# Kernel tuning notes

Hardware: AMD Instinct MI355X
Metric: run time of the kernel (lower is better)

The kernel has to match this reference:

```python
import jax, jax.numpy as jnp
import numpy as np

T, B, IN, H, OUT = 512, 128, 64, 1024, 64


def _gru_layer(x, w_ih, w_hh, b_ih, b_hh):
    # x: (T, B, in_dim); w_ih: (3H, in_dim); w_hh: (3H, H); gate order: r, z, n (torch)
    gi = jnp.einsum('tbi,gi->tbg', x, w_ih) + b_ih  # (T, B, 3H) input-side gates, precomputed
    h0 = jnp.zeros((x.shape[1], w_hh.shape[1]), x.dtype)

    def step(h, gi_t):
        gh = h @ w_hh.T + b_hh                      # (B, 3H)
        ir, iz, inn = jnp.split(gi_t, 3, axis=-1)
        hr, hz, hn = jnp.split(gh, 3, axis=-1)
        r = jax.nn.sigmoid(ir + hr)
        z = jax.nn.sigmoid(iz + hz)
        n = jnp.tanh(inn + r * hn)
        h_new = (1.0 - z) * n + z * h
        return h_new, h_new

    _, out = jax.lax.scan(step, h0, gi)             # out: (T, B, H)
    return out


def setup_inputs() -> dict:
    key = jax.random.key(0)
    ks = jax.random.split(key, 11)
    s_in = 1.0 / np.sqrt(H)
    inp = {
        'x': jax.random.normal(ks[0], (T, B, IN), dtype=jnp.float32),
        'w_ih0': jax.random.uniform(ks[1], (3 * H, IN), jnp.float32, -s_in, s_in),
        'w_hh0': jax.random.uniform(ks[2], (3 * H, H), jnp.float32, -s_in, s_in),
        'b_ih0': jax.random.uniform(ks[3], (3 * H,), jnp.float32, -s_in, s_in),
        'b_hh0': jax.random.uniform(ks[4], (3 * H,), jnp.float32, -s_in, s_in),
        'w_ih1': jax.random.uniform(ks[5], (3 * H, H), jnp.float32, -s_in, s_in),
        'w_hh1': jax.random.uniform(ks[6], (3 * H, H), jnp.float32, -s_in, s_in),
        'b_ih1': jax.random.uniform(ks[7], (3 * H,), jnp.float32, -s_in, s_in),
        'b_hh1': jax.random.uniform(ks[8], (3 * H,), jnp.float32, -s_in, s_in),
        'w_lin': jax.random.uniform(ks[9], (OUT, H), jnp.float32, -s_in, s_in),
        'b_lin': jax.random.uniform(ks[10], (OUT,), jnp.float32, -s_in, s_in),
    }
    return inp


def reference(x, w_ih0, w_hh0, b_ih0, b_hh0, w_ih1, w_hh1, b_ih1, b_hh1, w_lin, b_lin):
    h1 = _gru_layer(x, w_ih0, w_hh0, b_ih0, b_hh0)   # (T, B, H)
    h2 = _gru_layer(h1, w_ih1, w_hh1, b_ih1, b_hh1)  # (T, B, H)
    out = jnp.einsum('tbh,oh->tbo', h2, w_lin) + b_lin  # time-distributed linear
    return out
```

## Files before the change

kernel.cpp:

```cpp
#include <hip/hip_runtime.h>

#define Tn  512
#define Bn  128
#define INn 64
#define Hn  1024

typedef __attribute__((ext_vector_type(8))) _Float16 f16x8;
typedef __attribute__((ext_vector_type(4))) float f32x4;
typedef unsigned short u16;

#define AGENT __HIP_MEMORY_SCOPE_AGENT

__device__ __forceinline__ u16 f2h(float f) {
  union { _Float16 h; u16 u; } v;
  v.h = (_Float16)f;
  return v.u;
}
__device__ __forceinline__ float sigmoidf_(float x) {
  return 1.0f / (1.0f + __expf(-x));
}
__device__ __forceinline__ float tanhf_(float x) {
  float e = __expf(-2.0f * fabsf(x));
  float t = (1.0f - e) / (1.0f + e);
  return copysignf(t, x);
}
__device__ __forceinline__ f32x4 mfma16(f16x8 a, f16x8 b, f32x4 c) {
  return __builtin_amdgcn_mfma_f32_16x16x32_f16(a, b, c, 0, 0, 0);
}
__device__ __forceinline__ size_t hidx(int row, int col) {
  return ((size_t)((row >> 4) * 32 + (col >> 5))) * 512 +
         ((((col >> 3) & 3) * 16 + (row & 15)) * 8) + (col & 7);
}
__device__ __forceinline__ void acq_fence() {
  __builtin_amdgcn_fence(__ATOMIC_ACQUIRE, "agent");
}
__device__ __forceinline__ void coh_store(u16* p, u16 a, u16 b) {
  __hip_atomic_store((unsigned*)p, (unsigned)a | ((unsigned)b << 16),
                     __ATOMIC_RELAXED, AGENT);
}
__device__ __forceinline__ void ldb4(f16x8 dst[4], const u16* __restrict__ h,
                                     size_t ab, int kc0) {
#pragma unroll
  for (int k = 0; k < 4; ++k)
    dst[k] = *(const f16x8*)(h + ab + (size_t)(kc0 + k) * 512);
}
__device__ __forceinline__ void fma12(f32x4 acc[3], const f16x8 b[4],
                                      const f16x8 W[3][8], int kc0) {
#pragma unroll
  for (int k = 0; k < 4; ++k) {
#pragma unroll
    for (int g = 0; g < 3; ++g)
      acc[g] = mfma16(b[k], W[g][kc0 + k], acc[g]);
  }
}

__global__ void pack_w(const float* __restrict__ s, u16* __restrict__ d, int R, int K) {
  int tid = blockIdx.x * blockDim.x + threadIdx.x;
  int total = (R * K) >> 3;
  if (tid >= total) return;
  int l = tid & 63;
  int ckc = tid >> 6;
  int nkc = K >> 5;
  int ct = ckc / nkc;
  int kc = ckc - ct * nkc;
  int row = ct * 16 + (l & 15);
  int k0 = kc * 32 + (l >> 4) * 8;
  const float* sp = s + (size_t)row * K + k0;
  float4 a = *(const float4*)sp;
  float4 b = *(const float4*)(sp + 4);
  f16x8 o;
  u16* op = (u16*)&o;
  op[0] = f2h(a.x); op[1] = f2h(a.y); op[2] = f2h(a.z); op[3] = f2h(a.w);
  op[4] = f2h(b.x); op[5] = f2h(b.y); op[6] = f2h(b.z); op[7] = f2h(b.w);
  *(f16x8*)(d + (size_t)tid * 8) = o;
}

__global__ void zero16(uint4* __restrict__ p, int n4) {
  int i = blockIdx.x * blockDim.x + threadIdx.x;
  if (i < n4) p[i] = make_uint4(0u, 0u, 0u, 0u);
}

#define PS 131072

template <bool WO>
__global__ __launch_bounds__(512, 1) void gru_main(
    const float* __restrict__ x,
    const float* __restrict__ b_ih0, const float* __restrict__ b_hh0,
    const float* __restrict__ b_ih1, const float* __restrict__ b_hh1,
    const float* __restrict__ b_lin,
    const u16* __restrict__ wih0p, const u16* __restrict__ whh0p,
    const u16* __restrict__ wih1p, const u16* __restrict__ whh1p,
    const u16* __restrict__ wlinp,
    u16* __restrict__ hA, u16* __restrict__ hB,
    float* __restrict__ out, int* __restrict__ flags) {
  extern __shared__ float lds[];

  const int blk  = blockIdx.x;
  const int tid  = threadIdx.x;
  const int w    = tid >> 6;
  const int lane = tid & 63;
  const int ln   = lane & 15;
  const int lq   = lane >> 4;
  const int layer = blk >> 7;
  const int lb   = blk & 127;
  const f32x4 vz = {0.f, 0.f, 0.f, 0.f};

  if (layer == 0) {
    const int bg  = lb >> 5;
    const int hsl = lb & 31;
    const int q   = w & 1;
    const int kg  = w >> 1;
    const int c16 = hsl * 2 + q;
    const bool kgl = (kg < 2);
    const int xm  = kg;
    f16x8 W[3][8];
#pragma unroll
    for (int g = 0; g < 3; ++g)
#pragma unroll
      for (int kc = 0; kc < 8; ++kc)
        W[g][kc] = *(const f16x8*)(whh0p + (((size_t)(g * 64 + c16) * 32 + kg * 8 + kc) * 64 + lane) * 8);
    f16x8 Wx[3][2];
    if (kgl) {
#pragma unroll
      for (int g = 0; g < 3; ++g)
#pragma unroll
        for (int kc = 0; kc < 2; ++kc)
          Wx[g][kc] = *(const f16x8*)(wih0p + (((size_t)(g * 64 + c16) * 2 + kc) * 64 + lane) * 8);
    }
    const bool is_lin = (hsl < 8);
    const int lcg = hsl & 3;
    const int lrt = hsl >> 2;
    float Blin = 0.f;
    f16x8 Wl[4];
    if (is_lin) {
      Blin = b_lin[lcg * 16 + (tid & 15)];
#pragma unroll
      for (int kc = 0; kc < 4; ++kc)
        Wl[kc] = *(const f16x8*)(wlinp + (((size_t)lcg * 32 + w * 4 + kc) * 64 + lane) * 8);
    }
    const int rm  = tid >> 8;
    const int rr  = (tid >> 4) & 15;
    const int rc2 = (tid & 15) * 2;
    const int ggr = bg * 32 + rm * 16 + rr;
    float Br[2], Bz[2], Bni[2], Bnh[2];
#pragma unroll
    for (int e = 0; e < 2; ++e) {
      const int gc = hsl * 32 + rc2 + e;
      Br[e]  = b_ih0[gc] + b_hh0[gc];
      Bz[e]  = b_ih0[Hn + gc] + b_hh0[Hn + gc];
      Bni[e] = b_ih0[2 * Hn + gc];
      Bnh[e] = b_hh0[2 * Hn + gc];
    }
    const int* pPeer = flags + ((bg << 5) + (lane & 31)) * 32;
    const int* pBp   = flags + 4096 + (((bg >> 1) << 6) + lane) * 32;
    const size_t abL = ((size_t)(bg * 2 + lrt) * 32 + w * 4) * 512 + lane * 8;
    float h0prev[2] = {0.f, 0.f};

    for (int t = 0; t <= Tn + 7; ++t) {
      f16x8 lbuf[4];
      if (t < Tn) {
        if (w == 0) {
          const bool needB = WO ? (is_lin && t >= 8) : (t >= 8);
          for (;;) {
            bool ok = true;
            if (t > 0 && __hip_atomic_load(pPeer, __ATOMIC_RELAXED, AGENT) < t) ok = false;
            if (needB && __hip_atomic_load(pBp, __ATOMIC_RELAXED, AGENT) < t - 7) ok = false;
            if (!__all(ok)) { __builtin_amdgcn_s_sleep(1); continue; }
            break;
          }
          if (!WO) acq_fence();
        }
        __syncthreads();
        const u16* Ahb = hA + (size_t)(WO ? t : ((t + 7) & 7)) * PS;
        float4 xv0, xv1, xv2, xv3;
        if (kgl) {
          const float* xr = x + ((size_t)t * Bn + bg * 32 + xm * 16 + ln) * INn + lq * 8;
          xv0 = *(const float4*)xr;        xv1 = *(const float4*)(xr + 4);
          xv2 = *(const float4*)(xr + 32); xv3 = *(const float4*)(xr + 36);
        }
        f32x4 acc0[3] = {vz, vz, vz}, acc1[3] = {vz, vz, vz};
        f16x8 b0[4], b1[4], b2[4], b3[4];
        const size_t ab0 = ((size_t)(bg * 2 + 0) * 32 + kg * 8) * 512 + lane * 8;
        const size_t ab1 = ((size_t)(bg * 2 + 1) * 32 + kg * 8) * 512 + lane * 8;
        ldb4(b0, Ahb, ab0, 0);
        ldb4(b1, Ahb, ab0, 4);
        ldb4(b2, Ahb, ab1, 0);
        ldb4(b3, Ahb, ab1, 4);
        if (is_lin && t >= 8)
          ldb4(lbuf, hB + (size_t)(WO ? (t - 7) : ((t - 8) & 7)) * PS, abL, 0);
        fma12(acc0, b0, W, 0);
        fma12(acc0, b1, W, 4);
        fma12(acc1, b2, W, 0);
        fma12(acc1, b3, W, 4);
        {
          float* Hp0 = lds + (size_t)(0 * 4 + kg) * 1680;
          float* Hp1 = lds + (size_t)(1 * 4 + kg) * 1680;
#pragma unroll
          for (int g = 0; g < 3; ++g)
#pragma unroll
            for (int i = 0; i < 4; ++i) {
              Hp0[g * 560 + (lq * 4 + i) * 35 + q * 16 + ln] = acc0[g][i];
              Hp1[g * 560 + (lq * 4 + i) * 35 + q * 16 + ln] = acc1[g][i];
            }
        }
        if (kgl) {
          f16x8 a0, a1;
          u16* a0p = (u16*)&a0;
          u16* a1p = (u16*)&a1;
          a0p[0] = f2h(xv0.x); a0p[1] = f2h(xv0.y); a0p[2] = f2h(xv0.z); a0p[3] = f2h(xv0.w);
          a0p[4] = f2h(xv1.x); a0p[5] = f2h(xv1.y); a0p[6] = f2h(xv1.z); a0p[7] = f2h(xv1.w);
          a1p[0] = f2h(xv2.x); a1p[1] = f2h(xv2.y); a1p[2] = f2h(xv2.z); a1p[3] = f2h(xv2.w);
          a1p[4] = f2h(xv3.x); a1p[5] = f2h(xv3.y); a1p[6] = f2h(xv3.z); a1p[7] = f2h(xv3.w);
          f32x4 ax[3] = {vz, vz, vz};
#pragma unroll
          for (int g = 0; g < 3; ++g) {
            ax[g] = mfma16(a0, Wx[g][0], ax[g]);
            ax[g] = mfma16(a1, Wx[g][1], ax[g]);
          }
          float* Ip = lds + 13440 + (size_t)xm * 1680;
#pragma unroll
          for (int g = 0; g < 3; ++g)
#pragma unroll
            for (int i = 0; i < 4; ++i)
              Ip[g * 560 + (lq * 4 + i) * 35 + q * 16 + ln] = ax[g][i];
        }
        __syncthreads();
        {
          u16* whp = hA + (size_t)(WO ? (t + 1) : (t & 7)) * PS;
          const size_t idx0 = hidx(ggr, hsl * 32 + rc2);
          u16 hh[2];
#pragma unroll
          for (int e = 0; e < 2; ++e) {
            const int c = rc2 + e;
            const float* Ip = lds + 13440 + (size_t)rm * 1680 + rr * 35 + c;
            float I0 = Ip[0], I1 = Ip[560], I2 = Ip[1120];
            float H0 = 0.f, H1 = 0.f, H2 = 0.f;
#pragma unroll
            for (int kgi = 0; kgi < 4; ++kgi) {
              const float* Hp = lds + (size_t)(rm * 4 + kgi) * 1680 + rr * 35 + c;
              H0 += Hp[0]; H1 += Hp[560]; H2 += Hp[1120];
            }
            float r  = sigmoidf_(I0 + H0 + Br[e]);
            float zz = sigmoidf_(I1 + H1 + Bz[e]);
            float nn = tanhf_(I2 + Bni[e] + r * (H2 + Bnh[e]));
            float hv = (1.0f - zz) * nn + zz * h0prev[e];
            h0prev[e] = hv;
            hh[e] = f2h(hv);
          }
          coh_store(whp + idx0, hh[0], hh[1]);
        }
        __syncthreads();
        if (tid == 0)
          __hip_atomic_store(flags + ((bg << 5) + hsl) * 32, t + 1, __ATOMIC_RELAXED, AGENT);
      } else if (is_lin) {
        if (w == 0) {
          while (!__all(__hip_atomic_load(pBp, __ATOMIC_RELAXED, AGENT) >= t - 7))
            __builtin_amdgcn_s_sleep(1);
          if (!WO) acq_fence();
        }
        __syncthreads();
        ldb4(lbuf, hB + (size_t)(WO ? (t - 7) : ((t - 8) & 7)) * PS, abL, 0);
      }
      if (is_lin && t >= 8) {
        const int s2 = t - 8;
        f32x4 la = vz;
#pragma unroll
        for (int k = 0; k < 4; ++k)
          la = mfma16(lbuf[k], Wl[k], la);
        __syncthreads();
        if (!WO && tid == 0)
          __hip_atomic_store(flags + 8192 + ((bg << 3) + hsl) * 32, s2 + 1, __ATOMIC_RELAXED, AGENT);
#pragma unroll
        for (int i = 0; i < 4; ++i)
          lds[(w * 16 + lq * 4 + i) * 21 + ln] = la[i];
        __syncthreads();
        if (tid < 256) {
          const int lr = (tid >> 4) & 15, lc = tid & 15;
          float s = Blin;
#pragma unroll
          for (int w8 = 0; w8 < 8; ++w8)
            s += lds[(w8 * 16 + lr) * 21 + lc];
          out[((size_t)s2 * Bn + bg * 32 + lrt * 16 + lr) * 64 + lcg * 16 + lc] = s;
        }
      }
    }
  } else {
    const int cs  = lb >> 1;
    const int rh  = lb & 1;
    const int side = w >> 2;
    const int ks  = w & 3;
    const u16* wsrc = side ? whh1p : wih1p;
    f16x8 W[3][8];
#pragma unroll
    for (int g = 0; g < 3; ++g)
#pragma unroll
      for (int kc = 0; kc < 8; ++kc)
        W[g][kc] = *(const f16x8*)(wsrc + (((size_t)(g * 64 + cs) * 32 + ks * 8 + kc) * 64 + lane) * 8);
    const int mq  = tid >> 7;
    const int er  = (tid >> 3) & 15;
    const int ec0 = (tid & 7) * 2;
    float Br2[2], Bz2[2], Bni2[2], Bnh2[2];
#pragma unroll
    for (int e = 0; e < 2; ++e) {
      const int g2 = cs * 16 + ec0 + e;
      Br2[e]  = b_ih1[g2] + b_hh1[g2];
      Bz2[e]  = b_ih1[Hn + g2] + b_hh1[Hn + g2];
      Bni2[e] = b_ih1[2 * Hn + g2];
      Bnh2[e] = b_hh1[2 * Hn + g2];
    }
    const size_t idxE = hidx(rh * 64 + mq * 16 + er, cs * 16 + ec0);
    float h1prev[2] = {0.f, 0.f};
    const int* pA = flags + ((rh << 6) + lane) * 32;
    const int* pB = flags + 4096 + ((rh << 6) + lane) * 32;
    const int* pC = flags + 8192 + ((rh << 4) + (lane & 15)) * 32;

    for (int s = 0; s < Tn; ++s) {
      if (w == 0) {
        for (;;) {
          bool ok = __hip_atomic_load(pA, __ATOMIC_RELAXED, AGENT) >= s + 1;
          if (!WO && s >= 8 && (lane & 15) == lane &&
              __hip_atomic_load(pC, __ATOMIC_RELAXED, AGENT) < s - 7) ok = false;
          if (__all(ok)) break;
          __builtin_amdgcn_s_sleep(1);
        }
        if (!WO) acq_fence();
      }
      __syncthreads();
      const u16* A1h = hA + (size_t)(WO ? (s + 1) : (s & 7)) * PS;
      const u16* A2h = hB + (size_t)(WO ? s : ((s + 7) & 7)) * PS;
      u16* whp = hB + (size_t)(WO ? (s + 1) : (s & 7)) * PS;
      const u16* Ahb = side ? A2h : A1h;
      if (side && s > 0) {
        while (!__all(__hip_atomic_load(pB, __ATOMIC_RELAXED, AGENT) >= s))
          __builtin_amdgcn_s_sleep(1);
      }
      f32x4 acc0[3] = {vz, vz, vz}, acc1[3] = {vz, vz, vz};
      f32x4 acc2[3] = {vz, vz, vz}, acc3[3] = {vz, vz, vz};
      f16x8 b0[4], b1[4], b2[4], b3[4];
      const int mA = rh * 4;
      const size_t abT0 = ((size_t)(mA + 0) * 32 + ks * 8) * 512 + lane * 8;
      const size_t abT1 = ((size_t)(mA + 1) * 32 + ks * 8) * 512 + lane * 8;
      const size_t abT2 = ((size_t)(mA + 2) * 32 + ks * 8) * 512 + lane * 8;
      const size_t abT3 = ((size_t)(mA + 3) * 32 + ks * 8) * 512 + lane * 8;
      ldb4(b0, Ahb, abT0, 0);
      ldb4(b1, Ahb, abT0, 4);
      ldb4(b2, Ahb, abT1, 0);
      ldb4(b3, Ahb, abT1, 4);
      fma12(acc0, b0, W, 0);
      ldb4(b0, Ahb, abT2, 0);
      fma12(acc0, b1, W, 4);
      ldb4(b1, Ahb, abT2, 4);
      fma12(acc1, b2, W, 0);
      ldb4(b2, Ahb, abT3, 0);
      fma12(acc1, b3, W, 4);
      ldb4(b3, Ahb, abT3, 4);
      fma12(acc2, b0, W, 0);
      fma12(acc2, b1, W, 4);
      fma12(acc3, b2, W, 0);
      fma12(acc3, b3, W, 4);
#pragma unroll
      for (int g = 0; g < 3; ++g)
#pragma unroll
        for (int i = 0; i < 4; ++i) {
          const int ro = (lq * 4 + i) * 21 + ln;
          lds[((0 * 8 + w) * 3 + g) * 336 + ro] = acc0[g][i];
          lds[((1 * 8 + w) * 3 + g) * 336 + ro] = acc1[g][i];
          lds[((2 * 8 + w) * 3 + g) * 336 + ro] = acc2[g][i];
          lds[((3 * 8 + w) * 3 + g) * 336 + ro] = acc3[g][i];
        }
      __syncthreads();
      {
        u16 hh[2];
#pragma unroll
        for (int e = 0; e < 2; ++e) {
          const int rc = ec0 + e;
          float I0 = 0.f, I1 = 0.f, I2 = 0.f, H0 = 0.f, H1 = 0.f, H2 = 0.f;
#pragma unroll
          for (int wi = 0; wi < 4; ++wi) {
            const float* P = lds + ((mq * 8 + wi) * 3) * 336 + er * 21 + rc;
            I0 += P[0]; I1 += P[336]; I2 += P[672];
          }
#pragma unroll
          for (int wi = 4; wi < 8; ++wi) {
            const float* P = lds + ((mq * 8 + wi) * 3) * 336 + er * 21 + rc;
            H0 += P[0]; H1 += P[336]; H2 += P[672];
          }
          float r  = sigmoidf_(I0 + H0 + Br2[e]);
          float zz = sigmoidf_(I1 + H1 + Bz2[e]);
          float nn = tanhf_(I2 + Bni2[e] + r * (H2 + Bnh2[e]));
          float hv = (1.0f - zz) * nn + zz * h1prev[e];
          h1prev[e] = hv;
          hh[e] = f2h(hv);
        }
        coh_store(whp + idxE, hh[0], hh[1]);
      }
      __syncthreads();
      if (tid == 0)
        __hip_atomic_store(flags + 4096 + ((rh << 6) + cs) * 32, s + 1, __ATOMIC_RELAXED, AGENT);
    }
  }
}

extern "C" void kernel_launch(void* const* d_in, const int* in_sizes, int n_in,
                              void* d_out, int out_size, void* d_ws, size_t ws_size,
                              hipStream_t stream) {
  (void)in_sizes; (void)n_in; (void)out_size;
  const float* x     = (const float*)d_in[0];
  const float* wih0f = (const float*)d_in[1];
  const float* whh0f = (const float*)d_in[2];
  const float* bih0  = (const float*)d_in[3];
  const float* bhh0  = (const float*)d_in[4];
  const float* wih1f = (const float*)d_in[5];
  const float* whh1f = (const float*)d_in[6];
  const float* bih1  = (const float*)d_in[7];
  const float* bhh1  = (const float*)d_in[8];
  const float* wlinf = (const float*)d_in[9];
  const float* blin  = (const float*)d_in[10];
  float* out = (float*)d_out;

  const size_t wbytes = (size_t)3 * 3072 * 1024 * 2 + (size_t)3072 * 64 * 2 +
                        (size_t)64 * 1024 * 2;
  const size_t woNeed = wbytes + (size_t)2 * (Tn + 1) * PS * 2 + 36864;
  bool wo = (ws_size >= woNeed);
  const int planes = wo ? (Tn + 1) : 8;

  char* w = (char*)d_ws;
  u16* whh0p = (u16*)w; w += (size_t)3072 * 1024 * 2;
  u16* wih1p = (u16*)w; w += (size_t)3072 * 1024 * 2;
  u16* whh1p = (u16*)w; w += (size_t)3072 * 1024 * 2;
  u16* wih0p = (u16*)w; w += (size_t)3072 * 64 * 2;
  u16* wlinp = (u16*)w; w += (size_t)64 * 1024 * 2;
  u16* hA    = (u16*)w; w += (size_t)planes * PS * 2;
  u16* hB    = (u16*)w; w += (size_t)planes * PS * 2;
  int* flags = (int*)w; w += 36864;

  if (wo) {
    if (hipFuncSetAttribute((const void*)gru_main<true>,
                            hipFuncAttributeMaxDynamicSharedMemorySize,
                            131072) != hipSuccess)
      wo = false;
  }
  if (!wo) {
    (void)hipFuncSetAttribute((const void*)gru_main<false>,
                              hipFuncAttributeMaxDynamicSharedMemorySize, 131072);
  }

  const int thr = 256;
  pack_w<<<(3072 * 1024 / 8 + thr - 1) / thr, thr, 0, stream>>>(whh0f, whh0p, 3072, 1024);
  pack_w<<<(3072 * 1024 / 8 + thr - 1) / thr, thr, 0, stream>>>(wih1f, wih1p, 3072, 1024);
  pack_w<<<(3072 * 1024 / 8 + thr - 1) / thr, thr, 0, stream>>>(whh1f, whh1p, 3072, 1024);
  pack_w<<<(3072 * 64 / 8 + thr - 1) / thr, thr, 0, stream>>>(wih0f, wih0p, 3072, 64);
  pack_w<<<(64 * 1024 / 8 + thr - 1) / thr, thr, 0, stream>>>(wlinf, wlinp, 64, 1024);
  const int zplanes = wo ? 1 : 8;
  const int nzr = zplanes * PS * 2 / 16;
  zero16<<<(nzr + thr - 1) / thr, thr, 0, stream>>>((uint4*)hA, nzr);
  zero16<<<(nzr + thr - 1) / thr, thr, 0, stream>>>((uint4*)hB, nzr);
  zero16<<<(36864 / 16 + thr - 1) / thr, thr, 0, stream>>>((uint4*)flags, 36864 / 16);

  void* args[] = {(void*)&x,     (void*)&bih0,  (void*)&bhh0,  (void*)&bih1,  (void*)&bhh1,
                  (void*)&blin,  (void*)&wih0p, (void*)&whh0p, (void*)&wih1p, (void*)&whh1p,
                  (void*)&wlinp, (void*)&hA,    (void*)&hB,    (void*)&out,   (void*)&flags};
  const void* kfn = wo ? (const void*)gru_main<true> : (const void*)gru_main<false>;
  hipLaunchCooperativeKernel(kfn, dim3(256), dim3(512), args, 129024, stream);
}
```

Measured before the change: 4.088 ms.

## Use a ring of D hidden-state planes with periodic acquire fences

Replaces the write-once path (one plane per timestep) and the 8-plane ring with a ring of D planes (64, 16 or 8, chosen by workspace size), templated on depth and fence interval. Back-pressure flags are now always checked, at a depth of D-1 steps, and the acquire fence runs only every FI steps instead of every step. This shrinks the hidden-state buffer footprint so it can stay cache-resident, and cuts fence overhead. In exchange it adds reuse-distance flag checks, and correctness relies on skipped fences still giving enough visibility for the ring slots.

```diff
diff --git a/kernel.cpp b/kernel.cpp
--- a/kernel.cpp
+++ b/kernel.cpp
@@ -82,7 +82,7 @@
 
 #define PS 131072
 
-template <bool WO>
+template <int D, int FI>
 __global__ __launch_bounds__(512, 1) void gru_main(
     const float* __restrict__ x,
     const float* __restrict__ b_ih0, const float* __restrict__ b_hh0,
@@ -160,18 +160,19 @@
       f16x8 lbuf[4];
       if (t < Tn) {
         if (w == 0) {
-          const bool needB = WO ? (is_lin && t >= 8) : (t >= 8);
+          const bool needB = (is_lin && t >= 8) || (t >= D);
+          const int  thrB  = (is_lin && t >= 8) ? (t - 7) : (t - (D - 1));
           for (;;) {
             bool ok = true;
             if (t > 0 && __hip_atomic_load(pPeer, __ATOMIC_RELAXED, AGENT) < t) ok = false;
-            if (needB && __hip_atomic_load(pBp, __ATOMIC_RELAXED, AGENT) < t - 7) ok = false;
+            if (needB && __hip_atomic_load(pBp, __ATOMIC_RELAXED, AGENT) < thrB) ok = false;
             if (!__all(ok)) { __builtin_amdgcn_s_sleep(1); continue; }
             break;
           }
-          if (!WO) acq_fence();
-        }
-        __syncthreads();
-        const u16* Ahb = hA + (size_t)(WO ? t : ((t + 7) & 7)) * PS;
+          if ((t & (FI - 1)) == 0) acq_fence();
+        }
+        __syncthreads();
+        const u16* Ahb = hA + (size_t)((t + D - 1) & (D - 1)) * PS;
         float4 xv0, xv1, xv2, xv3;
         if (kgl) {
           const float* xr = x + ((size_t)t * Bn + bg * 32 + xm * 16 + ln) * INn + lq * 8;
@@ -187,7 +188,7 @@
         ldb4(b2, Ahb, ab1, 0);
         ldb4(b3, Ahb, ab1, 4);
         if (is_lin && t >= 8)
-          ldb4(lbuf, hB + (size_t)(WO ? (t - 7) : ((t - 8) & 7)) * PS, abL, 0);
+          ldb4(lbuf, hB + (size_t)((t - 8) & (D - 1)) * PS, abL, 0);
         fma12(acc0, b0, W, 0);
         fma12(acc0, b1, W, 4);
         fma12(acc1, b2, W, 0);
@@ -226,7 +227,7 @@
         }
         __syncthreads();
         {
-          u16* whp = hA + (size_t)(WO ? (t + 1) : (t & 7)) * PS;
+          u16* whp = hA + (size_t)(t & (D - 1)) * PS;
           const size_t idx0 = hidx(ggr, hsl * 32 + rc2);
           u16 hh[2];
 #pragma unroll
@@ -256,10 +257,10 @@
         if (w == 0) {
           while (!__all(__hip_atomic_load(pBp, __ATOMIC_RELAXED, AGENT) >= t - 7))
             __builtin_amdgcn_s_sleep(1);
-          if (!WO) acq_fence();
-        }
-        __syncthreads();
-        ldb4(lbuf, hB + (size_t)(WO ? (t - 7) : ((t - 8) & 7)) * PS, abL, 0);
+          if ((t & (FI - 1)) == 0) acq_fence();
+        }
+        __syncthreads();
+        ldb4(lbuf, hB + (size_t)((t - 8) & (D - 1)) * PS, abL, 0);
       }
       if (is_lin && t >= 8) {
         const int s2 = t - 8;
@@ -268,7 +269,7 @@
         for (int k = 0; k < 4; ++k)
           la = mfma16(lbuf[k], Wl[k], la);
         __syncthreads();
-        if (!WO && tid == 0)
+        if (tid == 0)
           __hip_atomic_store(flags + 8192 + ((bg << 3) + hsl) * 32, s2 + 1, __ATOMIC_RELAXED, AGENT);
 #pragma unroll
         for (int i = 0; i < 4; ++i)
@@ -318,17 +319,17 @@
       if (w == 0) {
         for (;;) {
           bool ok = __hip_atomic_load(pA, __ATOMIC_RELAXED, AGENT) >= s + 1;
-          if (!WO && s >= 8 && (lane & 15) == lane &&
-              __hip_atomic_load(pC, __ATOMIC_RELAXED, AGENT) < s - 7) ok = false;
+          if (s >= D && (lane & 15) == lane &&
+              __hip_atomic_load(pC, __ATOMIC_RELAXED, AGENT) < s - (D - 1)) ok = false;
           if (__all(ok)) break;
           __builtin_amdgcn_s_sleep(1);
         }
-        if (!WO) acq_fence();
+        if ((s & (FI - 1)) == 0) acq_fence();
       }
       __syncthreads();
-      const u16* A1h = hA + (size_t)(WO ? (s + 1) : (s & 7)) * PS;
-      const u16* A2h = hB + (size_t)(WO ? s : ((s + 7) & 7)) * PS;
-      u16* whp = hB + (size_t)(WO ? (s + 1) : (s & 7)) * PS;
+      const u16* A1h = hA + (size_t)(s & (D - 1)) * PS;
+      const u16* A2h = hB + (size_t)((s + D - 1) & (D - 1)) * PS;
+      u16* whp = hB + (size_t)(s & (D - 1)) * PS;
       const u16* Ahb = side ? A2h : A1h;
       if (side && s > 0) {
         while (!__all(__hip_atomic_load(pB, __ATOMIC_RELAXED, AGENT) >= s))
@@ -420,9 +421,9 @@
 
   const size_t wbytes = (size_t)3 * 3072 * 1024 * 2 + (size_t)3072 * 64 * 2 +
                         (size_t)64 * 1024 * 2;
-  const size_t woNeed = wbytes + (size_t)2 * (Tn + 1) * PS * 2 + 36864;
-  bool wo = (ws_size >= woNeed);
-  const int planes = wo ? (Tn + 1) : 8;
+  const size_t need64 = wbytes + (size_t)2 * 64 * PS * 2 + 36864;
+  const size_t need16 = wbytes + (size_t)2 * 16 * PS * 2 + 36864;
+  const int D = (ws_size >= need64) ? 64 : (ws_size >= need16 ? 16 : 8);
 
   char* w = (char*)d_ws;
   u16* whh0p = (u16*)w; w += (size_t)3072 * 1024 * 2;
@@ -430,20 +431,14 @@
   u16* whh1p = (u16*)w; w += (size_t)3072 * 1024 * 2;
   u16* wih0p = (u16*)w; w += (size_t)3072 * 64 * 2;
   u16* wlinp = (u16*)w; w += (size_t)64 * 1024 * 2;
-  u16* hA    = (u16*)w; w += (size_t)planes * PS * 2;
-  u16* hB    = (u16*)w; w += (size_t)planes * PS * 2;
+  u16* hA    = (u16*)w; w += (size_t)D * PS * 2;
+  u16* hB    = (u16*)w; w += (size_t)D * PS * 2;
   int* flags = (int*)w; w += 36864;
 
-  if (wo) {
-    if (hipFuncSetAttribute((const void*)gru_main<true>,
-                            hipFuncAttributeMaxDynamicSharedMemorySize,
-                            131072) != hipSuccess)
-      wo = false;
-  }
-  if (!wo) {
-    (void)hipFuncSetAttribute((const void*)gru_main<false>,
-                              hipFuncAttributeMaxDynamicSharedMemorySize, 131072);
-  }
+  const void* kfn = (D == 64) ? (const void*)gru_main<64, 32>
+                  : (D == 16) ? (const void*)gru_main<16, 8>
+                              : (const void*)gru_main<8, 1>;
+  (void)hipFuncSetAttribute(kfn, hipFuncAttributeMaxDynamicSharedMemorySize, 131072);
 
   const int thr = 256;
   pack_w<<<(3072 * 1024 / 8 + thr - 1) / thr, thr, 0, stream>>>(whh0f, whh0p, 3072, 1024);
@@ -451,8 +446,7 @@
   pack_w<<<(3072 * 1024 / 8 + thr - 1) / thr, thr, 0, stream>>>(whh1f, whh1p, 3072, 1024);
   pack_w<<<(3072 * 64 / 8 + thr - 1) / thr, thr, 0, stream>>>(wih0f, wih0p, 3072, 64);
   pack_w<<<(64 * 1024 / 8 + thr - 1) / thr, thr, 0, stream>>>(wlinf, wlinp, 64, 1024);
-  const int zplanes = wo ? 1 : 8;
-  const int nzr = zplanes * PS * 2 / 16;
+  const int nzr = D * PS * 2 / 16;
   zero16<<<(nzr + thr - 1) / thr, thr, 0, stream>>>((uint4*)hA, nzr);
   zero16<<<(nzr + thr - 1) / thr, thr, 0, stream>>>((uint4*)hB, nzr);
   zero16<<<(36864 / 16 + thr - 1) / thr, thr, 0, stream>>>((uint4*)flags, 36864 / 16);
@@ -460,6 +454,5 @@
   void* args[] = {(void*)&x,     (void*)&bih0,  (void*)&bhh0,  (void*)&bih1,  (void*)&bhh1,
                   (void*)&blin,  (void*)&wih0p, (void*)&whh0p, (void*)&wih1p, (void*)&whh1p,
                   (void*)&wlinp, (void*)&hA,    (void*)&hB,    (void*)&out,   (void*)&flags};
-  const void* kfn = wo ? (const void*)gru_main<true> : (const void*)gru_main<false>;
   hipLaunchCooperativeKernel(kfn, dim3(256), dim3(512), args, 129024, stream);
 }
```

Result: faster. 3.657 ms (-10.6%).
